# Optimization experiments

Measured on AMD Instinct MI355X. Metric: run time of the kernel, lower is better.

## Reference

```python
import jax, jax.numpy as jnp
import numpy as np

N_WIRES = 16
N_LAYERS = 4
BATCH = 256
DIM = 2 ** N_WIRES


def _rot_u(theta):
    # theta: (3,) = (rx, ry, rz) angles. Combined single-qubit unitary
    # U = RZ(rz) @ RY(ry) @ RX(rx), matching the gate application order
    # RX -> RY -> RZ in the circuit.
    a, b, c = theta[0] * 0.5, theta[1] * 0.5, theta[2] * 0.5
    cx = jnp.cos(a).astype(jnp.complex64)
    sx = jnp.sin(a).astype(jnp.complex64)
    cy = jnp.cos(b).astype(jnp.complex64)
    sy = jnp.sin(b).astype(jnp.complex64)
    RX = jnp.stack([jnp.stack([cx, -1j * sx]), jnp.stack([-1j * sx, cx])])
    RY = jnp.stack([jnp.stack([cy, -sy]), jnp.stack([sy, cy])])
    ez = jnp.exp(-1j * c.astype(jnp.complex64))
    RZ = jnp.stack([jnp.stack([ez, 0 * ez]), jnp.stack([0 * ez, jnp.conj(ez)])])
    return RZ @ (RY @ RX)


def _apply_1q(psi, U, q):
    # psi: [B] + [2]*n ; apply 2x2 unitary U on qubit axis q
    psi = jnp.moveaxis(psi, 1 + q, -1)
    psi = psi @ U.T  # new[i] = sum_j U[i,j] psi[j]
    return jnp.moveaxis(psi, -1, 1 + q)


def _apply_cnot(psi, c, t):
    # control qubit c, target qubit t
    psi = jnp.moveaxis(psi, (1 + c, 1 + t), (-2, -1))  # [..., 2(c), 2(t)]
    psi = jnp.stack([psi[..., 0, :], psi[..., 1, ::-1]], axis=-2)
    return jnp.moveaxis(psi, (-2, -1), (1 + c, 1 + t))


def _forward(state_batch, params, w_head, b_head):
    B = state_batch.shape[0]
    psi = state_batch.astype(jnp.complex64).reshape((B,) + (2,) * N_WIRES)
    # Precompute all fused RZ*RY*RX unitaries: [L, n, 2, 2]
    Us = jax.vmap(jax.vmap(_rot_u))(params)
    for layer in range(N_LAYERS):
        for q in range(N_WIRES):
            psi = _apply_1q(psi, Us[layer, q], q)
        for q in range(N_WIRES - 1):
            psi = _apply_cnot(psi, q, q + 1)
    psi = psi.reshape(B, DIM)
    probs = psi.real ** 2 + psi.imag ** 2  # [B, DIM], float32
    # PauliZ expectation per wire; wire 0 is the most significant bit
    idx = jnp.arange(DIM)[:, None]
    bits = (idx >> (N_WIRES - 1 - jnp.arange(N_WIRES))) & 1  # [DIM, n]
    signs = (1 - 2 * bits).astype(jnp.float32)
    features = probs @ signs  # [B, n]
    out = features @ w_head.T + b_head  # [B, 1]
    return out[:, 0]


def setup_inputs() -> dict:
    key = jax.random.key(0)
    k1, k2, k3, k4 = jax.random.split(key, 4)
    state = jax.random.normal(k1, (BATCH, DIM), jnp.float32)
    state = state / jnp.linalg.norm(state, axis=-1, keepdims=True)
    params = jax.random.normal(k2, (N_LAYERS, N_WIRES, 3), jnp.float32)
    w_head = jax.random.normal(k3, (1, N_WIRES), jnp.float32) / np.float32(np.sqrt(N_WIRES))
    b_head = jax.random.normal(k4, (1,), jnp.float32) * 0.01
    return {"state_batch": state, "params": params, "w_head": w_head, "b_head": b_head}


def reference(state_batch, params, w_head, b_head):
    return _forward(state_batch, params, w_head, b_head)
```

## Files before the change

### kernel.cpp

```cpp
#include <hip/hip_runtime.h>

typedef float v2f __attribute__((ext_vector_type(2)));

#define NT 256
#define NR 16

__device__ __forceinline__ int swz(int l) { return l ^ ((l >> 5) & 31); }

__device__ __forceinline__ void rot2(v2f& x, v2f& y, v2f aa, v2f an, v2f bb, v2f bn) {
  v2f xs = __builtin_shufflevector(x, x, 1, 0);
  v2f ys = __builtin_shufflevector(y, y, 1, 0);
  v2f n0 = aa * x + an * xs + bb * y + bn * ys;
  v2f n1 = aa * y - an * ys + bn * xs - bb * x;
  x = n0;
  y = n1;
}

#define ROT(T, G)                                                              \
  do {                                                                         \
    const float4 u = Utab[G];                                                  \
    const v2f aa = {u.x, u.x}, an = {-u.y, u.y};                               \
    const v2f bb = {u.z, u.z}, bn = {-u.w, u.w};                               \
    _Pragma("unroll") for (int v = 0; v < NR; ++v) if (!((v >> (T)) & 1))      \
        rot2(s[v], s[v | (1 << (T))], aa, an, bb, bn);                         \
  } while (0)

#define CNOTW(C, T)                                                            \
  do {                                                                         \
    _Pragma("unroll") for (int v = 0; v < NR; ++v)                             \
        if (((v >> (C)) & 1) && !((v >> (T)) & 1)) {                           \
      v2f tmp = s[v];                                                          \
      s[v] = s[v | (1 << (T))];                                                \
      s[v | (1 << (T))] = tmp;                                                 \
    }                                                                          \
  } while (0)

#define MAP_W1(t, v)  (((v) << 8) | (t))
#define MAP_W2(t, v)  ((((t) >> 5) << 9) | ((v) << 5) | ((t) & 31))
#define MAP_W3(t, v)  ((((t) >> 2) << 6) | ((v) << 2) | ((t) & 3))
#define MAP_W4(t, v)  (((t) << 4) | (v))
#define MAP_B3(t, v)  ((((t) >> 1) << 5) | ((v) << 1) | ((t) & 1))
#define MAP_C4(t, v)  ((((t) >> 4) << 8) | ((v) << 4) | ((t) & 15))
#define MAP_D63(t, v) ((((t) >> 3) << 7) | ((v) << 3) | ((t) & 7))

#define REMAP_W(MW)                                                            \
  _Pragma("unroll") for (int r = 0; r < NR; ++r) lds2[swz(MW(tid, r))] = s[r]
#define REMAP_R(MR)                                                            \
  _Pragma("unroll") for (int v = 0; v < NR; ++v) s[v] = lds2[swz(MR(tid, v))]

#define REMAP_L(MW, MR)  do { REMAP_W(MW); REMAP_R(MR); } while (0)
#define REMAP_BWB(MW, MR) do { __syncthreads(); REMAP_W(MW); __syncthreads(); REMAP_R(MR); } while (0)
#define REMAP_WB(MW, MR)  do { REMAP_W(MW); __syncthreads(); REMAP_R(MR); } while (0)

__global__ void k_setup(const float* __restrict__ params, float4* __restrict__ Utab) {
  int g = threadIdx.x;
  if (g < 64) {
    float a = params[g * 3 + 0] * 0.5f;
    float b = params[g * 3 + 1] * 0.5f;
    float c = params[g * 3 + 2] * 0.5f;
    float sa, ca, sb, cb, sc, cc;
    sincosf(a, &sa, &ca);
    sincosf(b, &sb, &cb);
    sincosf(c, &sc, &cc);
    float X = cb * ca, Y = sb * sa;
    float Xp = -sb * ca, Yp = -cb * sa;
    Utab[g] = make_float4(cc * X + sc * Y, cc * Y - sc * X,
                          cc * Xp + sc * Yp, cc * Yp - sc * Xp);
  }
}

__global__ __launch_bounds__(NT, 5) void k_passA(const float* __restrict__ in,
                                                 const float4* __restrict__ Utab,
                                                 v2f* __restrict__ st) {
  __shared__ v2f lds2[4096];
  const int tid = threadIdx.x;
  const int xcd = blockIdx.x & 7;
  const int y = blockIdx.x >> 3;
  const int g = y & 15;
  const int b = xcd | ((y >> 4) << 3);
  const float* base = in + (size_t)b * 65536;

  v2f s[NR];
#pragma unroll
  for (int v = 0; v < NR; ++v) {
    float re = base[(v << 12) + (tid << 4) + g];
    s[v] = v2f{re, 0.0f};
  }

#pragma unroll
  for (int l = 0; l < 4; ++l) {
    ROT(3, l * 16 + 0); ROT(2, l * 16 + 1); ROT(1, l * 16 + 2); ROT(0, l * 16 + 3);
    CNOTW(3, 2); CNOTW(2, 1); CNOTW(1, 0);
    REMAP_BWB(MAP_W1, MAP_W2);
    ROT(2, l * 16 + 4); ROT(1, l * 16 + 5); ROT(0, l * 16 + 6);
    CNOTW(3, 2); CNOTW(2, 1); CNOTW(1, 0);
    REMAP_L(MAP_W2, MAP_W3);
    ROT(2, l * 16 + 7); ROT(1, l * 16 + 8);
    if (l <= 2) ROT(0, l * 16 + 9);
    CNOTW(3, 2); CNOTW(2, 1);
    if (l <= 2) CNOTW(1, 0);
    if (l <= 1) {
      REMAP_L(MAP_W3, MAP_W4);
      if (l == 0) { ROT(1, 10); ROT(0, 11); CNOTW(2, 1); CNOTW(1, 0); }
      else        { ROT(1, 16 + 10); CNOTW(2, 1); }
      REMAP_WB(MAP_W4, MAP_W1);
    } else if (l == 2) {
      REMAP_WB(MAP_W3, MAP_W1);
    }
  }

  REMAP_W(MAP_W3);
  __syncthreads();
  v2f* outp = st + (size_t)b * 65536 + ((g >> 1) << 13) + (g & 1);
#pragma unroll
  for (int k = 0; k < 16; ++k) {
    int m = (k << 8) | tid;
    outp[m << 1] = lds2[swz((k << 8) | tid)];
  }
}

__global__ __launch_bounds__(NT, 5) void k_passB(const v2f* __restrict__ st,
                                                 const float4* __restrict__ Utab,
                                                 float* __restrict__ partials) {
  __shared__ v2f lds2[4096];
  const int tid = threadIdx.x;
  const int b = blockIdx.x >> 4;
  const int h = blockIdx.x & 15;
  const float4* base4 = (const float4*)(st + (size_t)b * 65536);

  v2f s[NR];
#pragma unroll
  for (int g2 = 0; g2 < 8; ++g2) {
    float4 f = base4[(g2 << 12) + (h << 8) + tid];
    s[2 * g2]     = v2f{f.x, f.y};
    s[2 * g2 + 1] = v2f{f.z, f.w};
  }

  ROT(3, 12); ROT(2, 13); ROT(1, 14); ROT(0, 15);
  REMAP_L(MAP_W4, MAP_B3);
  CNOTW(3, 2); CNOTW(2, 1); CNOTW(1, 0);
  ROT(3, 16 + 11); ROT(2, 16 + 12); ROT(1, 16 + 13);
  REMAP_L(MAP_B3, MAP_W4);
  CNOTW(1, 0);
  ROT(1, 16 + 14); ROT(0, 16 + 15);
  REMAP_L(MAP_W4, MAP_C4);
  CNOTW(1, 0);
  ROT(1, 32 + 10);
  CNOTW(2, 1);
  ROT(2, 48 + 9);
  CNOTW(3, 2);
  REMAP_L(MAP_C4, MAP_D63);
  CNOTW(1, 0);
  ROT(1, 32 + 11);
  CNOTW(2, 1);
  ROT(2, 48 + 10);
  CNOTW(3, 2);
  REMAP_L(MAP_D63, MAP_W3);
  CNOTW(1, 0);
  ROT(1, 32 + 12);
  CNOTW(2, 1);
  ROT(2, 48 + 11);
  CNOTW(3, 2);
  REMAP_L(MAP_W3, MAP_B3);
  CNOTW(1, 0);
  ROT(1, 32 + 13);
  CNOTW(2, 1);
  ROT(2, 48 + 12);
  CNOTW(3, 2);
  REMAP_L(MAP_B3, MAP_W4);
  CNOTW(1, 0);
  ROT(1, 32 + 14); ROT(0, 32 + 15);
  CNOTW(2, 1); CNOTW(1, 0);
  ROT(2, 48 + 13); ROT(1, 48 + 14); ROT(0, 48 + 15);
  CNOTW(3, 2); CNOTW(2, 1); CNOTW(1, 0);

  float P = 0.f, f12 = 0.f, f13 = 0.f, f14 = 0.f, f15 = 0.f;
#pragma unroll
  for (int v = 0; v < NR; ++v) {
    float p = s[v][0] * s[v][0] + s[v][1] * s[v][1];
    P += p;
    f12 += ((v >> 3) & 1) ? -p : p;
    f13 += ((v >> 2) & 1) ? -p : p;
    f14 += ((v >> 1) & 1) ? -p : p;
    f15 += ((v >> 0) & 1) ? -p : p;
  }
  float vals[13];
  vals[0] = P;
#pragma unroll
  for (int q = 4; q <= 11; ++q)
    vals[q - 3] = ((tid >> (11 - q)) & 1) ? -P : P;
  vals[9] = f12; vals[10] = f13; vals[11] = f14; vals[12] = f15;

  const int lane = tid & 63, w = tid >> 6;
#pragma unroll
  for (int q = 0; q < 13; ++q) {
    float x = vals[q];
#pragma unroll
    for (int m = 1; m < 64; m <<= 1) x += __shfl_xor(x, m, 64);
    vals[q] = x;
  }
  __syncthreads();
  float* red = (float*)lds2;
  if (lane == 0) {
#pragma unroll
    for (int q = 0; q < 13; ++q) red[q * 4 + w] = vals[q];
  }
  __syncthreads();
  if (tid < 13) {
    float F = 0.f;
#pragma unroll
    for (int ww = 0; ww < 4; ++ww) F += red[tid * 4 + ww];
    float* pt = partials + (size_t)blockIdx.x * 16;
    if (tid == 0) {
      pt[0] = (h & 8) ? -F : F;
      pt[1] = (h & 4) ? -F : F;
      pt[2] = (h & 2) ? -F : F;
      pt[3] = (h & 1) ? -F : F;
    } else {
      pt[tid + 3] = F;
    }
  }
}

__global__ void k_head(const float* __restrict__ partials, const float* __restrict__ w,
                       const float* __restrict__ bh, float* __restrict__ out) {
  int b = threadIdx.x;
  float acc = bh[0];
  for (int q = 0; q < 16; ++q) {
    float F = 0.f;
    for (int hh = 0; hh < 16; ++hh) F += partials[(size_t)(b * 16 + hh) * 16 + q];
    acc += w[q] * F;
  }
  out[b] = acc;
}

extern "C" void kernel_launch(void* const* d_in, const int* in_sizes, int n_in,
                              void* d_out, int out_size, void* d_ws, size_t ws_size,
                              hipStream_t stream) {
  const float* state  = (const float*)d_in[0];
  const float* params = (const float*)d_in[1];
  const float* w_head = (const float*)d_in[2];
  const float* b_head = (const float*)d_in[3];
  float* out = (float*)d_out;

  char* ws = (char*)d_ws;
  v2f* st = (v2f*)ws;
  float4* Utab = (float4*)(ws + (size_t)134217728);
  float* partials = (float*)(ws + (size_t)134217728 + 1024);

  k_setup<<<1, 64, 0, stream>>>(params, Utab);
  k_passA<<<dim3(4096), dim3(NT), 0, stream>>>(state, Utab, st);
  k_passB<<<dim3(4096), dim3(NT), 0, stream>>>(st, Utab, partials);
  k_head<<<1, 256, 0, stream>>>(partials, w_head, b_head, out);
}
```

Before: 237.8 us.

## Process two state slices per block and interleave their LDS remaps with compute

New measurement: 239.3 us. About the same (+0.6%).

```diff
diff --git a/kernel.cpp b/kernel.cpp
--- a/kernel.cpp
+++ b/kernel.cpp
@@ -16,22 +16,22 @@
   y = n1;
 }
 
-#define ROT(T, G)                                                              \
+#define ROTS(S, T, G)                                                          \
   do {                                                                         \
     const float4 u = Utab[G];                                                  \
     const v2f aa = {u.x, u.x}, an = {-u.y, u.y};                               \
     const v2f bb = {u.z, u.z}, bn = {-u.w, u.w};                               \
     _Pragma("unroll") for (int v = 0; v < NR; ++v) if (!((v >> (T)) & 1))      \
-        rot2(s[v], s[v | (1 << (T))], aa, an, bb, bn);                         \
+        rot2(S[v], S[v | (1 << (T))], aa, an, bb, bn);                         \
   } while (0)
 
-#define CNOTW(C, T)                                                            \
+#define CNOTS(S, C, T)                                                         \
   do {                                                                         \
     _Pragma("unroll") for (int v = 0; v < NR; ++v)                             \
         if (((v >> (C)) & 1) && !((v >> (T)) & 1)) {                           \
-      v2f tmp = s[v];                                                          \
-      s[v] = s[v | (1 << (T))];                                                \
-      s[v | (1 << (T))] = tmp;                                                 \
+      v2f tmp = S[v];                                                          \
+      S[v] = S[v | (1 << (T))];                                                \
+      S[v | (1 << (T))] = tmp;                                                 \
     }                                                                          \
   } while (0)
 
@@ -43,14 +43,58 @@
 #define MAP_C4(t, v)  ((((t) >> 4) << 8) | ((v) << 4) | ((t) & 15))
 #define MAP_D63(t, v) ((((t) >> 3) << 7) | ((v) << 3) | ((t) & 7))
 
-#define REMAP_W(MW)                                                            \
-  _Pragma("unroll") for (int r = 0; r < NR; ++r) lds2[swz(MW(tid, r))] = s[r]
-#define REMAP_R(MR)                                                            \
-  _Pragma("unroll") for (int v = 0; v < NR; ++v) s[v] = lds2[swz(MR(tid, v))]
-
-#define REMAP_L(MW, MR)  do { REMAP_W(MW); REMAP_R(MR); } while (0)
-#define REMAP_BWB(MW, MR) do { __syncthreads(); REMAP_W(MW); __syncthreads(); REMAP_R(MR); } while (0)
-#define REMAP_WB(MW, MR)  do { REMAP_W(MW); __syncthreads(); REMAP_R(MR); } while (0)
+#define WM(S, L, M) _Pragma("unroll") for (int r = 0; r < NR; ++r) L[swz(M(tid, r))] = S[r]
+#define RM(S, L, M) _Pragma("unroll") for (int v = 0; v < NR; ++v) S[v] = L[swz(M(tid, v))]
+
+#define GA1(S, l)                                                              \
+  do { ROTS(S, 3, (l)*16 + 0); ROTS(S, 2, (l)*16 + 1); ROTS(S, 1, (l)*16 + 2); \
+       ROTS(S, 0, (l)*16 + 3); CNOTS(S, 3, 2); CNOTS(S, 2, 1); CNOTS(S, 1, 0); } while (0)
+#define GA2(S, l)                                                              \
+  do { ROTS(S, 2, (l)*16 + 4); ROTS(S, 1, (l)*16 + 5); ROTS(S, 0, (l)*16 + 6); \
+       CNOTS(S, 3, 2); CNOTS(S, 2, 1); CNOTS(S, 1, 0); } while (0)
+#define GA3(S, l)                                                              \
+  do { ROTS(S, 2, (l)*16 + 7); ROTS(S, 1, (l)*16 + 8);                         \
+       if ((l) <= 2) ROTS(S, 0, (l)*16 + 9);                                   \
+       CNOTS(S, 3, 2); CNOTS(S, 2, 1);                                         \
+       if ((l) <= 2) CNOTS(S, 1, 0); } while (0)
+#define GA4(S, l)                                                              \
+  do { if ((l) == 0) { ROTS(S, 1, 10); ROTS(S, 0, 11); CNOTS(S, 2, 1); CNOTS(S, 1, 0); } \
+       else          { ROTS(S, 1, 26); CNOTS(S, 2, 1); } } while (0)
+
+#define GPRE(S) do { ROTS(S,3,12); ROTS(S,2,13); ROTS(S,1,14); ROTS(S,0,15); } while (0)
+#define GQ0(S)  do { CNOTS(S,3,2); CNOTS(S,2,1); CNOTS(S,1,0);                 \
+                     ROTS(S,3,27); ROTS(S,2,28); ROTS(S,1,29); } while (0)
+#define GQ1(S)  do { CNOTS(S,1,0); ROTS(S,1,30); ROTS(S,0,31); } while (0)
+#define GD0(S)  do { CNOTS(S,1,0); ROTS(S,1,42); CNOTS(S,2,1); ROTS(S,2,57); CNOTS(S,3,2); } while (0)
+#define GD1(S)  do { CNOTS(S,1,0); ROTS(S,1,43); CNOTS(S,2,1); ROTS(S,2,58); CNOTS(S,3,2); } while (0)
+#define GD2(S)  do { CNOTS(S,1,0); ROTS(S,1,44); CNOTS(S,2,1); ROTS(S,2,59); CNOTS(S,3,2); } while (0)
+#define GD3(S)  do { CNOTS(S,1,0); ROTS(S,1,45); CNOTS(S,2,1); ROTS(S,2,60); CNOTS(S,3,2); } while (0)
+#define GD4(S)  do { CNOTS(S,1,0); ROTS(S,1,46); ROTS(S,0,47);                 \
+                     CNOTS(S,2,1); CNOTS(S,1,0);                               \
+                     ROTS(S,2,61); ROTS(S,1,62); ROTS(S,0,63);                 \
+                     CNOTS(S,3,2); CNOTS(S,2,1); CNOTS(S,1,0); } while (0)
+
+#define EPIV(S, VALS)                                                          \
+  do {                                                                         \
+    float P = 0.f, f12 = 0.f, f13 = 0.f, f14 = 0.f, f15 = 0.f;                 \
+    _Pragma("unroll") for (int v = 0; v < NR; ++v) {                           \
+      float p = S[v][0] * S[v][0] + S[v][1] * S[v][1];                         \
+      P += p;                                                                  \
+      f12 += ((v >> 3) & 1) ? -p : p;                                          \
+      f13 += ((v >> 2) & 1) ? -p : p;                                          \
+      f14 += ((v >> 1) & 1) ? -p : p;                                          \
+      f15 += ((v >> 0) & 1) ? -p : p;                                          \
+    }                                                                          \
+    VALS[0] = P;                                                               \
+    _Pragma("unroll") for (int q = 4; q <= 11; ++q)                            \
+      VALS[q - 3] = ((tid >> (11 - q)) & 1) ? -P : P;                          \
+    VALS[9] = f12; VALS[10] = f13; VALS[11] = f14; VALS[12] = f15;             \
+    _Pragma("unroll") for (int q = 0; q < 13; ++q) {                           \
+      float x = VALS[q];                                                       \
+      _Pragma("unroll") for (int m = 1; m < 64; m <<= 1) x += __shfl_xor(x, m, 64); \
+      VALS[q] = x;                                                             \
+    }                                                                          \
+  } while (0)
 
 __global__ void k_setup(const float* __restrict__ params, float4* __restrict__ Utab) {
   int g = threadIdx.x;
@@ -69,155 +113,152 @@
   }
 }
 
-__global__ __launch_bounds__(NT, 5) void k_passA(const float* __restrict__ in,
+__global__ __launch_bounds__(NT, 2) void k_passA(const float* __restrict__ in,
                                                  const float4* __restrict__ Utab,
-                                                 v2f* __restrict__ st) {
-  __shared__ v2f lds2[4096];
+                                                 float4* __restrict__ st) {
+  __shared__ v2f lds0[4096];
+  __shared__ v2f lds1[4096];
   const int tid = threadIdx.x;
   const int xcd = blockIdx.x & 7;
   const int y = blockIdx.x >> 3;
-  const int g = y & 15;
-  const int b = xcd | ((y >> 4) << 3);
-  const float* base = in + (size_t)b * 65536;
-
-  v2f s[NR];
+  const int j = y & 7;
+  const int b = xcd | ((y >> 3) << 3);
+  const float* base = in + (size_t)b * 65536 + 2 * j;
+
+  v2f s0[NR], s1[NR];
 #pragma unroll
   for (int v = 0; v < NR; ++v) {
-    float re = base[(v << 12) + (tid << 4) + g];
-    s[v] = v2f{re, 0.0f};
+    float2 f = *(const float2*)(base + (((v << 8) | tid) << 4));
+    s0[v] = v2f{f.x, 0.0f};
+    s1[v] = v2f{f.y, 0.0f};
   }
 
 #pragma unroll
   for (int l = 0; l < 4; ++l) {
-    ROT(3, l * 16 + 0); ROT(2, l * 16 + 1); ROT(1, l * 16 + 2); ROT(0, l * 16 + 3);
-    CNOTW(3, 2); CNOTW(2, 1); CNOTW(1, 0);
-    REMAP_BWB(MAP_W1, MAP_W2);
-    ROT(2, l * 16 + 4); ROT(1, l * 16 + 5); ROT(0, l * 16 + 6);
-    CNOTW(3, 2); CNOTW(2, 1); CNOTW(1, 0);
-    REMAP_L(MAP_W2, MAP_W3);
-    ROT(2, l * 16 + 7); ROT(1, l * 16 + 8);
-    if (l <= 2) ROT(0, l * 16 + 9);
-    CNOTW(3, 2); CNOTW(2, 1);
-    if (l <= 2) CNOTW(1, 0);
+    GA1(s0, l); GA1(s1, l);
+    __syncthreads();
+    WM(s0, lds0, MAP_W1); WM(s1, lds1, MAP_W1);
+    __syncthreads();
+    RM(s0, lds0, MAP_W2); GA2(s0, l);
+    WM(s0, lds0, MAP_W2);
+    RM(s1, lds1, MAP_W2); GA2(s1, l);
+    WM(s1, lds1, MAP_W2);
+    RM(s0, lds0, MAP_W3); GA3(s0, l);
     if (l <= 1) {
-      REMAP_L(MAP_W3, MAP_W4);
-      if (l == 0) { ROT(1, 10); ROT(0, 11); CNOTW(2, 1); CNOTW(1, 0); }
-      else        { ROT(1, 16 + 10); CNOTW(2, 1); }
-      REMAP_WB(MAP_W4, MAP_W1);
+      WM(s0, lds0, MAP_W3);
+      RM(s1, lds1, MAP_W3); GA3(s1, l);
+      WM(s1, lds1, MAP_W3);
+      RM(s0, lds0, MAP_W4); GA4(s0, l);
+      WM(s0, lds0, MAP_W4);
+      RM(s1, lds1, MAP_W4); GA4(s1, l);
+      WM(s1, lds1, MAP_W4);
+      __syncthreads();
+      RM(s0, lds0, MAP_W1); RM(s1, lds1, MAP_W1);
     } else if (l == 2) {
-      REMAP_WB(MAP_W3, MAP_W1);
+      WM(s0, lds0, MAP_W3);
+      RM(s1, lds1, MAP_W3); GA3(s1, l);
+      WM(s1, lds1, MAP_W3);
+      __syncthreads();
+      RM(s0, lds0, MAP_W1); RM(s1, lds1, MAP_W1);
+    } else {
+      RM(s1, lds1, MAP_W3); GA3(s1, l);
     }
   }
 
-  REMAP_W(MAP_W3);
+  WM(s0, lds0, MAP_W3); WM(s1, lds1, MAP_W3);
   __syncthreads();
-  v2f* outp = st + (size_t)b * 65536 + ((g >> 1) << 13) + (g & 1);
+  float4* outp = st + ((size_t)b << 15) + (j << 12);
 #pragma unroll
   for (int k = 0; k < 16; ++k) {
     int m = (k << 8) | tid;
-    outp[m << 1] = lds2[swz((k << 8) | tid)];
-  }
-}
-
-__global__ __launch_bounds__(NT, 5) void k_passB(const v2f* __restrict__ st,
+    v2f a = lds0[swz(m)], c = lds1[swz(m)];
+    outp[m] = make_float4(a[0], a[1], c[0], c[1]);
+  }
+}
+
+__global__ __launch_bounds__(NT, 2) void k_passB(const float4* __restrict__ st,
                                                  const float4* __restrict__ Utab,
                                                  float* __restrict__ partials) {
-  __shared__ v2f lds2[4096];
+  __shared__ v2f lds0[4096];
+  __shared__ v2f lds1[4096];
   const int tid = threadIdx.x;
-  const int b = blockIdx.x >> 4;
-  const int h = blockIdx.x & 15;
-  const float4* base4 = (const float4*)(st + (size_t)b * 65536);
-
-  v2f s[NR];
+  const int b = blockIdx.x >> 3;
+  const int i = blockIdx.x & 7;
+  const int h0 = 2 * i, h1 = 2 * i + 1;
+  const float4* base4 = st + ((size_t)b << 15);
+
+  v2f s0[NR], s1[NR];
 #pragma unroll
   for (int g2 = 0; g2 < 8; ++g2) {
-    float4 f = base4[(g2 << 12) + (h << 8) + tid];
-    s[2 * g2]     = v2f{f.x, f.y};
-    s[2 * g2 + 1] = v2f{f.z, f.w};
-  }
-
-  ROT(3, 12); ROT(2, 13); ROT(1, 14); ROT(0, 15);
-  REMAP_L(MAP_W4, MAP_B3);
-  CNOTW(3, 2); CNOTW(2, 1); CNOTW(1, 0);
-  ROT(3, 16 + 11); ROT(2, 16 + 12); ROT(1, 16 + 13);
-  REMAP_L(MAP_B3, MAP_W4);
-  CNOTW(1, 0);
-  ROT(1, 16 + 14); ROT(0, 16 + 15);
-  REMAP_L(MAP_W4, MAP_C4);
-  CNOTW(1, 0);
-  ROT(1, 32 + 10);
-  CNOTW(2, 1);
-  ROT(2, 48 + 9);
-  CNOTW(3, 2);
-  REMAP_L(MAP_C4, MAP_D63);
-  CNOTW(1, 0);
-  ROT(1, 32 + 11);
-  CNOTW(2, 1);
-  ROT(2, 48 + 10);
-  CNOTW(3, 2);
-  REMAP_L(MAP_D63, MAP_W3);
-  CNOTW(1, 0);
-  ROT(1, 32 + 12);
-  CNOTW(2, 1);
-  ROT(2, 48 + 11);
-  CNOTW(3, 2);
-  REMAP_L(MAP_W3, MAP_B3);
-  CNOTW(1, 0);
-  ROT(1, 32 + 13);
-  CNOTW(2, 1);
-  ROT(2, 48 + 12);
-  CNOTW(3, 2);
-  REMAP_L(MAP_B3, MAP_W4);
-  CNOTW(1, 0);
-  ROT(1, 32 + 14); ROT(0, 32 + 15);
-  CNOTW(2, 1); CNOTW(1, 0);
-  ROT(2, 48 + 13); ROT(1, 48 + 14); ROT(0, 48 + 15);
-  CNOTW(3, 2); CNOTW(2, 1); CNOTW(1, 0);
-
-  float P = 0.f, f12 = 0.f, f13 = 0.f, f14 = 0.f, f15 = 0.f;
-#pragma unroll
-  for (int v = 0; v < NR; ++v) {
-    float p = s[v][0] * s[v][0] + s[v][1] * s[v][1];
-    P += p;
-    f12 += ((v >> 3) & 1) ? -p : p;
-    f13 += ((v >> 2) & 1) ? -p : p;
-    f14 += ((v >> 1) & 1) ? -p : p;
-    f15 += ((v >> 0) & 1) ? -p : p;
-  }
-  float vals[13];
-  vals[0] = P;
-#pragma unroll
-  for (int q = 4; q <= 11; ++q)
-    vals[q - 3] = ((tid >> (11 - q)) & 1) ? -P : P;
-  vals[9] = f12; vals[10] = f13; vals[11] = f14; vals[12] = f15;
+    float4 f = base4[(g2 << 12) + (h0 << 8) + tid];
+    s0[2 * g2]     = v2f{f.x, f.y};
+    s0[2 * g2 + 1] = v2f{f.z, f.w};
+  }
+#pragma unroll
+  for (int g2 = 0; g2 < 8; ++g2) {
+    float4 f = base4[(g2 << 12) + (h1 << 8) + tid];
+    s1[2 * g2]     = v2f{f.x, f.y};
+    s1[2 * g2 + 1] = v2f{f.z, f.w};
+  }
+
+  GPRE(s0); WM(s0, lds0, MAP_W4);
+  GPRE(s1);
+  RM(s0, lds0, MAP_B3);  WM(s1, lds1, MAP_W4);
+  GQ0(s0);  WM(s0, lds0, MAP_B3);
+  RM(s1, lds1, MAP_B3);
+  GQ0(s1);
+  RM(s0, lds0, MAP_W4);  WM(s1, lds1, MAP_B3);
+  GQ1(s0);  WM(s0, lds0, MAP_W4);
+  RM(s1, lds1, MAP_W4);
+  GQ1(s1);
+  RM(s0, lds0, MAP_C4);  WM(s1, lds1, MAP_W4);
+  GD0(s0);  WM(s0, lds0, MAP_C4);
+  RM(s1, lds1, MAP_C4);
+  GD0(s1);
+  RM(s0, lds0, MAP_D63); WM(s1, lds1, MAP_C4);
+  GD1(s0);  WM(s0, lds0, MAP_D63);
+  RM(s1, lds1, MAP_D63);
+  GD1(s1);
+  RM(s0, lds0, MAP_W3);  WM(s1, lds1, MAP_D63);
+  GD2(s0);  WM(s0, lds0, MAP_W3);
+  RM(s1, lds1, MAP_W3);
+  GD2(s1);
+  RM(s0, lds0, MAP_B3);  WM(s1, lds1, MAP_W3);
+  GD3(s0);  WM(s0, lds0, MAP_B3);
+  RM(s1, lds1, MAP_B3);
+  GD3(s1);
+  RM(s0, lds0, MAP_W4);  WM(s1, lds1, MAP_B3);
+  GD4(s0);
+  RM(s1, lds1, MAP_W4);
+  GD4(s1);
+
+  float vals0[13], vals1[13];
+  EPIV(s0, vals0);
+  EPIV(s1, vals1);
 
   const int lane = tid & 63, w = tid >> 6;
-#pragma unroll
-  for (int q = 0; q < 13; ++q) {
-    float x = vals[q];
-#pragma unroll
-    for (int m = 1; m < 64; m <<= 1) x += __shfl_xor(x, m, 64);
-    vals[q] = x;
-  }
   __syncthreads();
-  float* red = (float*)lds2;
+  float* red0 = (float*)lds0;
+  float* red1 = (float*)lds1;
   if (lane == 0) {
 #pragma unroll
-    for (int q = 0; q < 13; ++q) red[q * 4 + w] = vals[q];
+    for (int q = 0; q < 13; ++q) { red0[q * 4 + w] = vals0[q]; red1[q * 4 + w] = vals1[q]; }
   }
   __syncthreads();
   if (tid < 13) {
-    float F = 0.f;
-#pragma unroll
-    for (int ww = 0; ww < 4; ++ww) F += red[tid * 4 + ww];
-    float* pt = partials + (size_t)blockIdx.x * 16;
+    float F0 = 0.f, F1 = 0.f;
+#pragma unroll
+    for (int ww = 0; ww < 4; ++ww) { F0 += red0[tid * 4 + ww]; F1 += red1[tid * 4 + ww]; }
+    float* pt0 = partials + ((size_t)(b * 16 + h0)) * 16;
+    float* pt1 = partials + ((size_t)(b * 16 + h1)) * 16;
     if (tid == 0) {
-      pt[0] = (h & 8) ? -F : F;
-      pt[1] = (h & 4) ? -F : F;
-      pt[2] = (h & 2) ? -F : F;
-      pt[3] = (h & 1) ? -F : F;
+      pt0[0] = (h0 & 8) ? -F0 : F0;  pt1[0] = (h1 & 8) ? -F1 : F1;
+      pt0[1] = (h0 & 4) ? -F0 : F0;  pt1[1] = (h1 & 4) ? -F1 : F1;
+      pt0[2] = (h0 & 2) ? -F0 : F0;  pt1[2] = (h1 & 2) ? -F1 : F1;
+      pt0[3] = (h0 & 1) ? -F0 : F0;  pt1[3] = (h1 & 1) ? -F1 : F1;
     } else {
-      pt[tid + 3] = F;
+      pt0[tid + 3] = F0;
+      pt1[tid + 3] = F1;
     }
   }
 }
@@ -244,12 +285,12 @@
   float* out = (float*)d_out;
 
   char* ws = (char*)d_ws;
-  v2f* st = (v2f*)ws;
+  float4* st = (float4*)ws;
   float4* Utab = (float4*)(ws + (size_t)134217728);
   float* partials = (float*)(ws + (size_t)134217728 + 1024);
 
   k_setup<<<1, 64, 0, stream>>>(params, Utab);
-  k_passA<<<dim3(4096), dim3(NT), 0, stream>>>(state, Utab, st);
-  k_passB<<<dim3(4096), dim3(NT), 0, stream>>>(st, Utab, partials);
+  k_passA<<<dim3(2048), dim3(NT), 0, stream>>>(state, Utab, st);
+  k_passB<<<dim3(2048), dim3(NT), 0, stream>>>(st, Utab, partials);
   k_head<<<1, 256, 0, stream>>>(partials, w_head, b_head, out);
 }
```
